# Performance work log

Measured on AMD Instinct MI355X. Metric: run time of the kernel, lower is better.

The kernel has to match this reference:

```python
import jax, jax.numpy as jnp
import numpy as np
import math

B, L, H, E = 4, 2048, 8, 64


def setup_inputs() -> dict:
    key = jax.random.key(0)
    kq, kk, kv, ks = jax.random.split(key, 4)
    return {
        "queries": jax.random.normal(kq, (B, L, H, E), dtype=jnp.float32),
        "keys": jax.random.normal(kk, (B, L, H, E), dtype=jnp.float32),
        "values": jax.random.normal(kv, (B, L, H, E), dtype=jnp.float32),
        "sigma": jax.random.normal(ks, (B, L, H), dtype=jnp.float32),
    }


def reference(queries, keys, values, sigma):
    Bq, Lq, Hq, Eq = queries.shape
    scale = 1.0 / math.sqrt(Eq)
    # QK^T: [B, H, L, S]
    scores = jnp.einsum("blhe,bshe->bhls", queries, keys)
    # triangular causal mask (mask_flag=True, attn_mask=None)
    causal = jnp.triu(jnp.ones((Lq, Lq), dtype=bool), k=1)
    scores = jnp.where(causal[None, None], -jnp.inf, scores)
    attn = scale * scores
    series = jax.nn.softmax(attn, axis=-1)  # dropout p=0.0 -> identity
    # sigma: [B, L, H] -> [B, H, L]
    sig = jnp.transpose(sigma, (0, 2, 1))
    sig = jax.nn.sigmoid(sig * 5.0) + 1e-5
    sig = jnp.power(3.0, sig) - 1.0
    sig = jnp.broadcast_to(sig[..., None], (Bq, Hq, Lq, Lq))  # [B,H,L,L]
    # |i - j| distances
    idx = jnp.arange(Lq, dtype=jnp.float32)
    dist = jnp.abs(idx[:, None] - idx[None, :])  # [L, L]
    prior = (1.0 / (math.sqrt(2.0 * math.pi) * sig)) * jnp.exp(
        -(dist[None, None] ** 2) / (2.0 * sig ** 2)
    )
    V = jnp.einsum("bhls,bshd->blhd", series, values)
    return V, series, prior, sig
```

## Files before the change

kernel.cpp:

```cpp
#include <hip/hip_runtime.h>
#include <math.h>

#define BB 4
#define LL 2048
#define HH 8
#define EE 64
#define TM 64
#define TN 64
#define SH 72

typedef _Float16 half4v __attribute__((ext_vector_type(4)));
typedef _Float16 half8v __attribute__((ext_vector_type(8)));
typedef float floatx4 __attribute__((ext_vector_type(4)));

static constexpr float SCALE = 0.125f;
static constexpr float LN3 = 1.0986122886681098f;
static constexpr float INV_SQRT_2PI = 0.3989422804014327f;
static constexpr size_t NMAT = (size_t)BB * HH * LL * LL;
static constexpr size_t SERIES_BASE = (size_t)BB * LL * HH * EE;
static constexpr size_t PRIOR_BASE = SERIES_BASE + NMAT;
static constexpr size_t SIG_BASE = PRIOR_BASE + NMAT;

__global__ __launch_bounds__(256, 8)
void prior_sig_fill(const float* __restrict__ sgg, float* __restrict__ out) {
  const int lane = threadIdx.x & 63;
  const int wv = (blockIdx.x << 2) | (threadIdx.x >> 6);
  const int nw = gridDim.x << 2;
  const int totalRows = BB * HH * LL;
  for (int row = wv; row < totalRows; row += nw) {
    const int bh = row >> 11;
    const int i = row & (LL - 1);
    const int b = bh >> 3, h = bh & 7;
    float sg = sgg[((size_t)b * LL + i) * HH + h];
    float sd = 1.0f / (1.0f + __expf(-5.0f * sg)) + 1e-5f;
    float sv = expm1f(sd * LN3);
    float iv = INV_SQRT_2PI / sv;
    float c2 = 0.5f / (sv * sv);
    const size_t roff = ((size_t)bh * LL + i) * LL;
    const floatx4 s4 = {sv, sv, sv, sv};
    const float fi = (float)i;
#pragma unroll
    for (int it = 0; it < 8; ++it) {
      int j = (it << 8) + (lane << 2);
      float d0 = fi - (float)j;
      float d1 = d0 - 1.0f, d2 = d0 - 2.0f, d3 = d0 - 3.0f;
      floatx4 pr;
      pr.x = iv * __expf(-d0 * d0 * c2);
      pr.y = iv * __expf(-d1 * d1 * c2);
      pr.z = iv * __expf(-d2 * d2 * c2);
      pr.w = iv * __expf(-d3 * d3 * c2);
      __builtin_nontemporal_store(pr, (floatx4*)&out[PRIOR_BASE + roff + j]);
      __builtin_nontemporal_store(s4, (floatx4*)&out[SIG_BASE + roff + j]);
    }
    const int jz = ((i >> 6) + 1) << 6;
    const floatx4 z = {0.f, 0.f, 0.f, 0.f};
    for (int j = jz + (lane << 2); j < LL; j += 256) {
      __builtin_nontemporal_store(z, (floatx4*)&out[SERIES_BASE + roff + j]);
    }
  }
}

__global__ __launch_bounds__(256, 2)
void anomaly_attn(const float* __restrict__ qg,
                  const float* __restrict__ kg,
                  const float* __restrict__ vg,
                  float* __restrict__ out) {
  __shared__ __attribute__((aligned(16))) _Float16 Qh[TM * SH];
  __shared__ __attribute__((aligned(16))) _Float16 Kh[TN * SH];
  __shared__ __attribute__((aligned(16))) _Float16 Vt[EE * SH];
  __shared__ __attribute__((aligned(16))) _Float16 Ph[TM * SH];

  const int t = threadIdx.x;
  const int lane = t & 63;
  const int w = t >> 6;
  const int quad = lane >> 4;
  const int l15 = lane & 15;
  const int bh = blockIdx.y;
  const int b = bh >> 3, h = bh & 7;
  const float4* q4 = (const float4*)qg;
  const float4* k4 = (const float4*)kg;
  const float4* v4 = (const float4*)vg;

  for (int half = 0; half < 2; ++half) {
    const int rt = half ? (31 - (int)blockIdx.x) : (int)blockIdx.x;
    const int i0 = rt * TM;
    const int nt = rt + 1;
    __syncthreads();

#pragma unroll
    for (int it = 0; it < 4; ++it) {
      int idx = t + 256 * it;
      int r = idx >> 4, c = idx & 15;
      float4 qv = q4[(((size_t)b * LL + i0 + r) * HH + h) * 16 + c];
      half4v hq = {(_Float16)qv.x, (_Float16)qv.y, (_Float16)qv.z, (_Float16)qv.w};
      *(half4v*)&Qh[r * SH + c * 4] = hq;
    }

    float lsum[4] = {0.f, 0.f, 0.f, 0.f};
    for (int jt = 0; jt < nt; ++jt) {
      const int j0 = jt * TN;
      __syncthreads();
#pragma unroll
      for (int it = 0; it < 4; ++it) {
        int idx = t + 256 * it;
        int r = idx >> 4, c = idx & 15;
        float4 kv = k4[(((size_t)b * LL + j0 + r) * HH + h) * 16 + c];
        half4v hk = {(_Float16)kv.x, (_Float16)kv.y, (_Float16)kv.z, (_Float16)kv.w};
        *(half4v*)&Kh[r * SH + c * 4] = hk;
      }
      __syncthreads();
      floatx4 acc[4] = {{0.f, 0.f, 0.f, 0.f}, {0.f, 0.f, 0.f, 0.f},
                        {0.f, 0.f, 0.f, 0.f}, {0.f, 0.f, 0.f, 0.f}};
#pragma unroll
      for (int ks = 0; ks < 2; ++ks) {
        half8v a = *(half8v*)&Qh[(w * 16 + l15) * SH + ks * 32 + quad * 8];
#pragma unroll
        for (int f = 0; f < 4; ++f) {
          half8v bf = *(half8v*)&Kh[(f * 16 + l15) * SH + ks * 32 + quad * 8];
          acc[f] = __builtin_amdgcn_mfma_f32_16x16x32_f16(a, bf, acc[f], 0, 0, 0);
        }
      }
#pragma unroll
      for (int f = 0; f < 4; ++f) {
        int j = j0 + f * 16 + l15;
#pragma unroll
        for (int r = 0; r < 4; ++r) {
          int i = i0 + w * 16 + quad * 4 + r;
          lsum[r] += (j <= i) ? __expf(acc[f][r] * SCALE) : 0.f;
        }
      }
    }
#pragma unroll
    for (int r = 0; r < 4; ++r) {
      lsum[r] += __shfl_xor(lsum[r], 1);
      lsum[r] += __shfl_xor(lsum[r], 2);
      lsum[r] += __shfl_xor(lsum[r], 4);
      lsum[r] += __shfl_xor(lsum[r], 8);
    }
    float linv[4];
#pragma unroll
    for (int r = 0; r < 4; ++r) linv[r] = 1.0f / lsum[r];

    floatx4 Oacc[4] = {{0.f, 0.f, 0.f, 0.f}, {0.f, 0.f, 0.f, 0.f},
                       {0.f, 0.f, 0.f, 0.f}, {0.f, 0.f, 0.f, 0.f}};
    for (int jt = 0; jt < nt; ++jt) {
      const int j0 = jt * TN;
      __syncthreads();
#pragma unroll
      for (int it = 0; it < 4; ++it) {
        int idx = t + 256 * it;
        int r = idx >> 4, c = idx & 15;
        float4 kv = k4[(((size_t)b * LL + j0 + r) * HH + h) * 16 + c];
        half4v hk = {(_Float16)kv.x, (_Float16)kv.y, (_Float16)kv.z, (_Float16)kv.w};
        *(half4v*)&Kh[r * SH + c * 4] = hk;
      }
      {
        const int tx = t & 15, ty = t >> 4;
        float4 vv[4];
#pragma unroll
        for (int rr = 0; rr < 4; ++rr)
          vv[rr] = v4[(((size_t)b * LL + j0 + ty * 4 + rr) * HH + h) * 16 + tx];
#pragma unroll
        for (int c = 0; c < 4; ++c) {
          float e0 = c == 0 ? vv[0].x : c == 1 ? vv[0].y : c == 2 ? vv[0].z : vv[0].w;
          float e1 = c == 0 ? vv[1].x : c == 1 ? vv[1].y : c == 2 ? vv[1].z : vv[1].w;
          float e2 = c == 0 ? vv[2].x : c == 1 ? vv[2].y : c == 2 ? vv[2].z : vv[2].w;
          float e3 = c == 0 ? vv[3].x : c == 1 ? vv[3].y : c == 2 ? vv[3].z : vv[3].w;
          half4v hv = {(_Float16)e0, (_Float16)e1, (_Float16)e2, (_Float16)e3};
          *(half4v*)&Vt[(tx * 4 + c) * SH + ty * 4] = hv;
        }
      }
      __syncthreads();
      floatx4 acc[4] = {{0.f, 0.f, 0.f, 0.f}, {0.f, 0.f, 0.f, 0.f},
                        {0.f, 0.f, 0.f, 0.f}, {0.f, 0.f, 0.f, 0.f}};
#pragma unroll
      for (int ks = 0; ks < 2; ++ks) {
        half8v a = *(half8v*)&Qh[(w * 16 + l15) * SH + ks * 32 + quad * 8];
#pragma unroll
        for (int f = 0; f < 4; ++f) {
          half8v bf = *(half8v*)&Kh[(f * 16 + l15) * SH + ks * 32 + quad * 8];
          acc[f] = __builtin_amdgcn_mfma_f32_16x16x32_f16(a, bf, acc[f], 0, 0, 0);
        }
      }
#pragma unroll
      for (int f = 0; f < 4; ++f) {
        int j = j0 + f * 16 + l15;
#pragma unroll
        for (int r = 0; r < 4; ++r) {
          int i = i0 + w * 16 + quad * 4 + r;
          float p = (j <= i) ? __expf(acc[f][r] * SCALE) * linv[r] : 0.f;
          Ph[(w * 16 + quad * 4 + r) * SH + f * 16 + l15] = (_Float16)p;
        }
      }
      __syncthreads();
#pragma unroll
      for (int rnd = 0; rnd < 2; ++rnd) {
        int idx = t + 256 * rnd;
        int r = idx >> 3, c8 = idx & 7;
        half8v p = *(half8v*)&Ph[r * SH + c8 * 8];
        floatx4 lo = {(float)p[0], (float)p[1], (float)p[2], (float)p[3]};
        floatx4 hi = {(float)p[4], (float)p[5], (float)p[6], (float)p[7]};
        size_t off = SERIES_BASE + ((size_t)bh * LL + i0 + r) * LL + j0 + c8 * 8;
        __builtin_nontemporal_store(lo, (floatx4*)&out[off]);
        __builtin_nontemporal_store(hi, (floatx4*)&out[off + 4]);
      }
#pragma unroll
      for (int ks = 0; ks < 2; ++ks) {
        half8v a = *(half8v*)&Ph[(w * 16 + l15) * SH + ks * 32 + quad * 8];
#pragma unroll
        for (int f = 0; f < 4; ++f) {
          half8v bv = *(half8v*)&Vt[(f * 16 + l15) * SH + ks * 32 + quad * 8];
          Oacc[f] = __builtin_amdgcn_mfma_f32_16x16x32_f16(a, bv, Oacc[f], 0, 0, 0);
        }
      }
    }
#pragma unroll
    for (int f = 0; f < 4; ++f) {
#pragma unroll
      for (int r = 0; r < 4; ++r) {
        int i = i0 + w * 16 + quad * 4 + r;
        out[(((size_t)b * LL + i) * HH + h) * EE + f * 16 + l15] = Oacc[f][r];
      }
    }
  }
}

extern "C" void kernel_launch(void* const* d_in, const int* in_sizes, int n_in,
                              void* d_out, int out_size, void* d_ws, size_t ws_size,
                              hipStream_t stream) {
  const float* q = (const float*)d_in[0];
  const float* k = (const float*)d_in[1];
  const float* v = (const float*)d_in[2];
  const float* sg = (const float*)d_in[3];
  float* out = (float*)d_out;
  prior_sig_fill<<<dim3(2048), 256, 0, stream>>>(sg, out);
  dim3 grid(LL / TM / 2, BB * HH);
  anomaly_attn<<<grid, 256, 0, stream>>>(q, k, v, out);
}
```

Baseline: 1.763 ms.

## Fuse two-pass softmax into single pass with deferred series normalization

Replaces the two-pass scheme, which recomputed QK^T once for row sums and again for probabilities, with a single pass. That pass accumulates row sums, writes unnormalized probabilities to the series output, and normalizes the PV accumulator at the end. A tail loop then reads the series rows back from global memory, scales them by the inverse row sum and stores them again. The kernel now launches one block per row tile instead of pairing tiles for load balance, raises the occupancy hint, and runs the prior fill after the attention kernel. This removes the duplicated QK matmul and exp work but adds a full read-modify-write of the causal half of the series matrix and loses the triangular load balancing.

```diff
diff --git a/kernel.cpp b/kernel.cpp
--- a/kernel.cpp
+++ b/kernel.cpp
@@ -60,7 +60,7 @@
   }
 }
 
-__global__ __launch_bounds__(256, 2)
+__global__ __launch_bounds__(256, 4)
 void anomaly_attn(const float* __restrict__ qg,
                   const float* __restrict__ kg,
                   const float* __restrict__ vg,
@@ -69,6 +69,7 @@
   __shared__ __attribute__((aligned(16))) _Float16 Kh[TN * SH];
   __shared__ __attribute__((aligned(16))) _Float16 Vt[EE * SH];
   __shared__ __attribute__((aligned(16))) _Float16 Ph[TM * SH];
+  __shared__ float s_linv[TM];
 
   const int t = threadIdx.x;
   const int lane = t & 63;
@@ -77,150 +78,136 @@
   const int l15 = lane & 15;
   const int bh = blockIdx.y;
   const int b = bh >> 3, h = bh & 7;
+  const int rt = blockIdx.x;
+  const int i0 = rt * TM;
+  const int nt = rt + 1;
   const float4* q4 = (const float4*)qg;
   const float4* k4 = (const float4*)kg;
   const float4* v4 = (const float4*)vg;
 
-  for (int half = 0; half < 2; ++half) {
-    const int rt = half ? (31 - (int)blockIdx.x) : (int)blockIdx.x;
-    const int i0 = rt * TM;
-    const int nt = rt + 1;
+#pragma unroll
+  for (int it = 0; it < 4; ++it) {
+    int idx = t + 256 * it;
+    int r = idx >> 4, c = idx & 15;
+    float4 qv = q4[(((size_t)b * LL + i0 + r) * HH + h) * 16 + c];
+    half4v hq = {(_Float16)qv.x, (_Float16)qv.y, (_Float16)qv.z, (_Float16)qv.w};
+    *(half4v*)&Qh[r * SH + c * 4] = hq;
+  }
+
+  float lsum[4] = {0.f, 0.f, 0.f, 0.f};
+  floatx4 Oacc[4] = {{0.f, 0.f, 0.f, 0.f}, {0.f, 0.f, 0.f, 0.f},
+                     {0.f, 0.f, 0.f, 0.f}, {0.f, 0.f, 0.f, 0.f}};
+
+  for (int jt = 0; jt < nt; ++jt) {
+    const int j0 = jt * TN;
     __syncthreads();
-
 #pragma unroll
     for (int it = 0; it < 4; ++it) {
       int idx = t + 256 * it;
       int r = idx >> 4, c = idx & 15;
-      float4 qv = q4[(((size_t)b * LL + i0 + r) * HH + h) * 16 + c];
-      half4v hq = {(_Float16)qv.x, (_Float16)qv.y, (_Float16)qv.z, (_Float16)qv.w};
-      *(half4v*)&Qh[r * SH + c * 4] = hq;
-    }
-
-    float lsum[4] = {0.f, 0.f, 0.f, 0.f};
-    for (int jt = 0; jt < nt; ++jt) {
-      const int j0 = jt * TN;
-      __syncthreads();
-#pragma unroll
-      for (int it = 0; it < 4; ++it) {
-        int idx = t + 256 * it;
-        int r = idx >> 4, c = idx & 15;
-        float4 kv = k4[(((size_t)b * LL + j0 + r) * HH + h) * 16 + c];
-        half4v hk = {(_Float16)kv.x, (_Float16)kv.y, (_Float16)kv.z, (_Float16)kv.w};
-        *(half4v*)&Kh[r * SH + c * 4] = hk;
-      }
-      __syncthreads();
-      floatx4 acc[4] = {{0.f, 0.f, 0.f, 0.f}, {0.f, 0.f, 0.f, 0.f},
-                        {0.f, 0.f, 0.f, 0.f}, {0.f, 0.f, 0.f, 0.f}};
-#pragma unroll
-      for (int ks = 0; ks < 2; ++ks) {
-        half8v a = *(half8v*)&Qh[(w * 16 + l15) * SH + ks * 32 + quad * 8];
-#pragma unroll
-        for (int f = 0; f < 4; ++f) {
-          half8v bf = *(half8v*)&Kh[(f * 16 + l15) * SH + ks * 32 + quad * 8];
-          acc[f] = __builtin_amdgcn_mfma_f32_16x16x32_f16(a, bf, acc[f], 0, 0, 0);
-        }
-      }
+      float4 kv = k4[(((size_t)b * LL + j0 + r) * HH + h) * 16 + c];
+      half4v hk = {(_Float16)kv.x, (_Float16)kv.y, (_Float16)kv.z, (_Float16)kv.w};
+      *(half4v*)&Kh[r * SH + c * 4] = hk;
+    }
+    {
+      const int tx = t & 15, ty = t >> 4;
+      float4 vv[4];
+#pragma unroll
+      for (int rr = 0; rr < 4; ++rr)
+        vv[rr] = v4[(((size_t)b * LL + j0 + ty * 4 + rr) * HH + h) * 16 + tx];
+#pragma unroll
+      for (int c = 0; c < 4; ++c) {
+        float e0 = c == 0 ? vv[0].x : c == 1 ? vv[0].y : c == 2 ? vv[0].z : vv[0].w;
+        float e1 = c == 0 ? vv[1].x : c == 1 ? vv[1].y : c == 2 ? vv[1].z : vv[1].w;
+        float e2 = c == 0 ? vv[2].x : c == 1 ? vv[2].y : c == 2 ? vv[2].z : vv[2].w;
+        float e3 = c == 0 ? vv[3].x : c == 1 ? vv[3].y : c == 2 ? vv[3].z : vv[3].w;
+        half4v hv = {(_Float16)e0, (_Float16)e1, (_Float16)e2, (_Float16)e3};
+        *(half4v*)&Vt[(tx * 4 + c) * SH + ty * 4] = hv;
+      }
+    }
+    __syncthreads();
+
+    floatx4 acc[4] = {{0.f, 0.f, 0.f, 0.f}, {0.f, 0.f, 0.f, 0.f},
+                      {0.f, 0.f, 0.f, 0.f}, {0.f, 0.f, 0.f, 0.f}};
+#pragma unroll
+    for (int ks = 0; ks < 2; ++ks) {
+      half8v a = *(half8v*)&Qh[(w * 16 + l15) * SH + ks * 32 + quad * 8];
 #pragma unroll
       for (int f = 0; f < 4; ++f) {
-        int j = j0 + f * 16 + l15;
-#pragma unroll
-        for (int r = 0; r < 4; ++r) {
-          int i = i0 + w * 16 + quad * 4 + r;
-          lsum[r] += (j <= i) ? __expf(acc[f][r] * SCALE) : 0.f;
-        }
-      }
-    }
-#pragma unroll
-    for (int r = 0; r < 4; ++r) {
-      lsum[r] += __shfl_xor(lsum[r], 1);
-      lsum[r] += __shfl_xor(lsum[r], 2);
-      lsum[r] += __shfl_xor(lsum[r], 4);
-      lsum[r] += __shfl_xor(lsum[r], 8);
-    }
-    float linv[4];
-#pragma unroll
-    for (int r = 0; r < 4; ++r) linv[r] = 1.0f / lsum[r];
-
-    floatx4 Oacc[4] = {{0.f, 0.f, 0.f, 0.f}, {0.f, 0.f, 0.f, 0.f},
-                       {0.f, 0.f, 0.f, 0.f}, {0.f, 0.f, 0.f, 0.f}};
-    for (int jt = 0; jt < nt; ++jt) {
-      const int j0 = jt * TN;
-      __syncthreads();
-#pragma unroll
-      for (int it = 0; it < 4; ++it) {
-        int idx = t + 256 * it;
-        int r = idx >> 4, c = idx & 15;
-        float4 kv = k4[(((size_t)b * LL + j0 + r) * HH + h) * 16 + c];
-        half4v hk = {(_Float16)kv.x, (_Float16)kv.y, (_Float16)kv.z, (_Float16)kv.w};
-        *(half4v*)&Kh[r * SH + c * 4] = hk;
-      }
-      {
-        const int tx = t & 15, ty = t >> 4;
-        float4 vv[4];
-#pragma unroll
-        for (int rr = 0; rr < 4; ++rr)
-          vv[rr] = v4[(((size_t)b * LL + j0 + ty * 4 + rr) * HH + h) * 16 + tx];
-#pragma unroll
-        for (int c = 0; c < 4; ++c) {
-          float e0 = c == 0 ? vv[0].x : c == 1 ? vv[0].y : c == 2 ? vv[0].z : vv[0].w;
-          float e1 = c == 0 ? vv[1].x : c == 1 ? vv[1].y : c == 2 ? vv[1].z : vv[1].w;
-          float e2 = c == 0 ? vv[2].x : c == 1 ? vv[2].y : c == 2 ? vv[2].z : vv[2].w;
-          float e3 = c == 0 ? vv[3].x : c == 1 ? vv[3].y : c == 2 ? vv[3].z : vv[3].w;
-          half4v hv = {(_Float16)e0, (_Float16)e1, (_Float16)e2, (_Float16)e3};
-          *(half4v*)&Vt[(tx * 4 + c) * SH + ty * 4] = hv;
-        }
-      }
-      __syncthreads();
-      floatx4 acc[4] = {{0.f, 0.f, 0.f, 0.f}, {0.f, 0.f, 0.f, 0.f},
-                        {0.f, 0.f, 0.f, 0.f}, {0.f, 0.f, 0.f, 0.f}};
-#pragma unroll
-      for (int ks = 0; ks < 2; ++ks) {
-        half8v a = *(half8v*)&Qh[(w * 16 + l15) * SH + ks * 32 + quad * 8];
-#pragma unroll
-        for (int f = 0; f < 4; ++f) {
-          half8v bf = *(half8v*)&Kh[(f * 16 + l15) * SH + ks * 32 + quad * 8];
-          acc[f] = __builtin_amdgcn_mfma_f32_16x16x32_f16(a, bf, acc[f], 0, 0, 0);
-        }
-      }
-#pragma unroll
-      for (int f = 0; f < 4; ++f) {
-        int j = j0 + f * 16 + l15;
-#pragma unroll
-        for (int r = 0; r < 4; ++r) {
-          int i = i0 + w * 16 + quad * 4 + r;
-          float p = (j <= i) ? __expf(acc[f][r] * SCALE) * linv[r] : 0.f;
-          Ph[(w * 16 + quad * 4 + r) * SH + f * 16 + l15] = (_Float16)p;
-        }
-      }
-      __syncthreads();
-#pragma unroll
-      for (int rnd = 0; rnd < 2; ++rnd) {
-        int idx = t + 256 * rnd;
-        int r = idx >> 3, c8 = idx & 7;
-        half8v p = *(half8v*)&Ph[r * SH + c8 * 8];
-        floatx4 lo = {(float)p[0], (float)p[1], (float)p[2], (float)p[3]};
-        floatx4 hi = {(float)p[4], (float)p[5], (float)p[6], (float)p[7]};
-        size_t off = SERIES_BASE + ((size_t)bh * LL + i0 + r) * LL + j0 + c8 * 8;
-        __builtin_nontemporal_store(lo, (floatx4*)&out[off]);
-        __builtin_nontemporal_store(hi, (floatx4*)&out[off + 4]);
-      }
-#pragma unroll
-      for (int ks = 0; ks < 2; ++ks) {
-        half8v a = *(half8v*)&Ph[(w * 16 + l15) * SH + ks * 32 + quad * 8];
-#pragma unroll
-        for (int f = 0; f < 4; ++f) {
-          half8v bv = *(half8v*)&Vt[(f * 16 + l15) * SH + ks * 32 + quad * 8];
-          Oacc[f] = __builtin_amdgcn_mfma_f32_16x16x32_f16(a, bv, Oacc[f], 0, 0, 0);
-        }
+        half8v bf = *(half8v*)&Kh[(f * 16 + l15) * SH + ks * 32 + quad * 8];
+        acc[f] = __builtin_amdgcn_mfma_f32_16x16x32_f16(a, bf, acc[f], 0, 0, 0);
       }
     }
 #pragma unroll
     for (int f = 0; f < 4; ++f) {
+      int j = j0 + f * 16 + l15;
 #pragma unroll
       for (int r = 0; r < 4; ++r) {
         int i = i0 + w * 16 + quad * 4 + r;
-        out[(((size_t)b * LL + i) * HH + h) * EE + f * 16 + l15] = Oacc[f][r];
-      }
+        float p = (j <= i) ? __expf(acc[f][r] * SCALE) : 0.f;
+        lsum[r] += p;
+        Ph[(w * 16 + quad * 4 + r) * SH + f * 16 + l15] = (_Float16)p;
+      }
+    }
+#pragma unroll
+    for (int rnd = 0; rnd < 2; ++rnd) {
+      int row = w * 16 + rnd * 8 + (lane >> 3);
+      int c8 = lane & 7;
+      half8v p = *(half8v*)&Ph[row * SH + c8 * 8];
+      floatx4 lo = {(float)p[0], (float)p[1], (float)p[2], (float)p[3]};
+      floatx4 hi = {(float)p[4], (float)p[5], (float)p[6], (float)p[7]};
+      size_t off = SERIES_BASE + ((size_t)bh * LL + i0 + row) * LL + j0 + c8 * 8;
+      *(floatx4*)&out[off] = lo;
+      *(floatx4*)&out[off + 4] = hi;
+    }
+#pragma unroll
+    for (int ks = 0; ks < 2; ++ks) {
+      half8v a = *(half8v*)&Ph[(w * 16 + l15) * SH + ks * 32 + quad * 8];
+#pragma unroll
+      for (int f = 0; f < 4; ++f) {
+        half8v bv = *(half8v*)&Vt[(f * 16 + l15) * SH + ks * 32 + quad * 8];
+        Oacc[f] = __builtin_amdgcn_mfma_f32_16x16x32_f16(a, bv, Oacc[f], 0, 0, 0);
+      }
+    }
+  }
+
+#pragma unroll
+  for (int r = 0; r < 4; ++r) {
+    lsum[r] += __shfl_xor(lsum[r], 1);
+    lsum[r] += __shfl_xor(lsum[r], 2);
+    lsum[r] += __shfl_xor(lsum[r], 4);
+    lsum[r] += __shfl_xor(lsum[r], 8);
+  }
+  float linv[4];
+#pragma unroll
+  for (int r = 0; r < 4; ++r) linv[r] = 1.0f / lsum[r];
+
+#pragma unroll
+  for (int f = 0; f < 4; ++f) {
+#pragma unroll
+    for (int r = 0; r < 4; ++r) {
+      int i = i0 + w * 16 + quad * 4 + r;
+      out[(((size_t)b * LL + i) * HH + h) * EE + f * 16 + l15] = Oacc[f][r] * linv[r];
+    }
+  }
+
+  if (l15 == 0) {
+#pragma unroll
+    for (int r = 0; r < 4; ++r) s_linv[w * 16 + quad * 4 + r] = linv[r];
+  }
+  __syncthreads();
+
+  const int ncol4 = nt * 16;
+  const int rsub = t >> 6;
+  const int cl = t & 63;
+  for (int rr = 0; rr < 16; ++rr) {
+    int row = rr * 4 + rsub;
+    float li = s_linv[row];
+    size_t base = SERIES_BASE + ((size_t)bh * LL + i0 + row) * LL;
+    for (int c = cl; c < ncol4; c += 64) {
+      floatx4 v = *(const floatx4*)&out[base + c * 4];
+      v *= li;
+      __builtin_nontemporal_store(v, (floatx4*)&out[base + c * 4]);
     }
   }
 }
@@ -233,7 +220,7 @@
   const float* v = (const float*)d_in[2];
   const float* sg = (const float*)d_in[3];
   float* out = (float*)d_out;
+  dim3 grid(LL / TM, BB * HH);
+  anomaly_attn<<<grid, 256, 0, stream>>>(q, k, v, out);
   prior_sig_fill<<<dim3(2048), 256, 0, stream>>>(sg, out);
-  dim3 grid(LL / TM / 2, BB * HH);
-  anomaly_attn<<<grid, 256, 0, stream>>>(q, k, v, out);
 }
```

Measured after the change: 1.920 ms. 8.9% more time.

## Fuse prior/sigma fill and series zero-fill into attention kernel

Applied to the files above, without the earlier changes.

Removes the separate prior_sig_fill launch and moves its work into the attention kernel. Each block computes per-row sigma constants into shared memory, then writes chunks of the prior, sigma and upper-triangle zero regions between its QK and PV tile iterations, with any leftover chunks written at the end. Block indices are remapped so each block owns one (b,h) pair and a complementary pair of row tiles. The intent is to overlap the large output store traffic with matrix compute, at the cost of more register and code pressure in the attention kernel and uneven store work per iteration.

```diff
diff --git a/kernel.cpp b/kernel.cpp
--- a/kernel.cpp
+++ b/kernel.cpp
@@ -21,68 +21,92 @@
 static constexpr size_t PRIOR_BASE = SERIES_BASE + NMAT;
 static constexpr size_t SIG_BASE = PRIOR_BASE + NMAT;
 
-__global__ __launch_bounds__(256, 8)
-void prior_sig_fill(const float* __restrict__ sgg, float* __restrict__ out) {
-  const int lane = threadIdx.x & 63;
-  const int wv = (blockIdx.x << 2) | (threadIdx.x >> 6);
-  const int nw = gridDim.x << 2;
-  const int totalRows = BB * HH * LL;
-  for (int row = wv; row < totalRows; row += nw) {
-    const int bh = row >> 11;
-    const int i = row & (LL - 1);
-    const int b = bh >> 3, h = bh & 7;
-    float sg = sgg[((size_t)b * LL + i) * HH + h];
-    float sd = 1.0f / (1.0f + __expf(-5.0f * sg)) + 1e-5f;
-    float sv = expm1f(sd * LN3);
-    float iv = INV_SQRT_2PI / sv;
-    float c2 = 0.5f / (sv * sv);
-    const size_t roff = ((size_t)bh * LL + i) * LL;
-    const floatx4 s4 = {sv, sv, sv, sv};
-    const float fi = (float)i;
-#pragma unroll
-    for (int it = 0; it < 8; ++it) {
-      int j = (it << 8) + (lane << 2);
-      float d0 = fi - (float)j;
-      float d1 = d0 - 1.0f, d2 = d0 - 2.0f, d3 = d0 - 3.0f;
-      floatx4 pr;
-      pr.x = iv * __expf(-d0 * d0 * c2);
-      pr.y = iv * __expf(-d1 * d1 * c2);
-      pr.z = iv * __expf(-d2 * d2 * c2);
-      pr.w = iv * __expf(-d3 * d3 * c2);
-      __builtin_nontemporal_store(pr, (floatx4*)&out[PRIOR_BASE + roff + j]);
-      __builtin_nontemporal_store(s4, (floatx4*)&out[SIG_BASE + roff + j]);
-    }
-    const int jz = ((i >> 6) + 1) << 6;
-    const floatx4 z = {0.f, 0.f, 0.f, 0.f};
-    for (int j = jz + (lane << 2); j < LL; j += 256) {
-      __builtin_nontemporal_store(z, (floatx4*)&out[SERIES_BASE + roff + j]);
-    }
-  }
-}
-
 __global__ __launch_bounds__(256, 2)
 void anomaly_attn(const float* __restrict__ qg,
                   const float* __restrict__ kg,
                   const float* __restrict__ vg,
+                  const float* __restrict__ sgg,
                   float* __restrict__ out) {
   __shared__ __attribute__((aligned(16))) _Float16 Qh[TM * SH];
   __shared__ __attribute__((aligned(16))) _Float16 Kh[TN * SH];
   __shared__ __attribute__((aligned(16))) _Float16 Vt[EE * SH];
   __shared__ __attribute__((aligned(16))) _Float16 Ph[TM * SH];
+  __shared__ float s_sigv[2 * TM], s_pinv[2 * TM], s_c2[2 * TM];
 
   const int t = threadIdx.x;
   const int lane = t & 63;
   const int w = t >> 6;
   const int quad = lane >> 4;
   const int l15 = lane & 15;
-  const int bh = blockIdx.y;
+
+  const int rx = blockIdx.x;
+  const int ry = blockIdx.y;
+  const int bh = (rx & 7) | ((ry & 3) << 3);
+  const int st = (rx >> 3) | ((ry >> 2) << 1);
   const int b = bh >> 3, h = bh & 7;
+  const int rt0 = st, rt1 = 31 - st;
+  const int i00 = rt0 * TM, i01 = rt1 * TM;
+
   const float4* q4 = (const float4*)qg;
   const float4* k4 = (const float4*)kg;
   const float4* v4 = (const float4*)vg;
 
+  if (t < 128) {
+    int hf = t >> 6, rr = t & 63;
+    int irow = (hf ? i01 : i00) + rr;
+    float sg = sgg[((size_t)b * LL + irow) * HH + h];
+    float sd = 1.0f / (1.0f + __expf(-5.0f * sg)) + 1e-5f;
+    float sv = expm1f(sd * LN3);
+    s_sigv[t] = sv;
+    s_pinv[t] = INV_SQRT_2PI / sv;
+    s_c2[t] = 0.5f / (sv * sv);
+  }
+
+  int cq = 0;
+  const int z0 = 31 - st;
+  auto write_chunk = [&](int c) {
+    if (c < 64) {
+      const int hf = c >> 5;
+      const int jc = c & 31;
+      const int i0c = hf ? i01 : i00;
+#pragma unroll
+      for (int u = 0; u < 4; ++u) {
+        int idx = t + 256 * u;
+        int rr = idx >> 4, cc = idx & 15;
+        int sidx = hf * 64 + rr;
+        float iv = s_pinv[sidx], c2 = s_c2[sidx], sv = s_sigv[sidx];
+        float fi = (float)(i0c + rr);
+        float d0 = fi - (float)(jc * 64 + cc * 4);
+        float d1 = d0 - 1.0f, d2 = d0 - 2.0f, d3 = d0 - 3.0f;
+        floatx4 pr;
+        pr.x = iv * __expf(-d0 * d0 * c2);
+        pr.y = iv * __expf(-d1 * d1 * c2);
+        pr.z = iv * __expf(-d2 * d2 * c2);
+        pr.w = iv * __expf(-d3 * d3 * c2);
+        size_t off = ((size_t)bh * LL + (i0c + rr)) * LL + jc * 64 + cc * 4;
+        __builtin_nontemporal_store(pr, (floatx4*)&out[PRIOR_BASE + off]);
+        floatx4 s4 = {sv, sv, sv, sv};
+        __builtin_nontemporal_store(s4, (floatx4*)&out[SIG_BASE + off]);
+      }
+    } else {
+      int z = c - 64;
+      int hf, jc;
+      if (z < z0) { hf = 0; jc = st + 1 + z; }
+      else        { hf = 1; jc = z + 1; }
+      const int i0c = hf ? i01 : i00;
+      const floatx4 zz = {0.f, 0.f, 0.f, 0.f};
+#pragma unroll
+      for (int u = 0; u < 4; ++u) {
+        int idx = t + 256 * u;
+        int rr = idx >> 4, cc = idx & 15;
+        size_t off = SERIES_BASE + ((size_t)bh * LL + (i0c + rr)) * LL + jc * 64 + cc * 4;
+        __builtin_nontemporal_store(zz, (floatx4*)&out[off]);
+      }
+    }
+  };
+
   for (int half = 0; half < 2; ++half) {
-    const int rt = half ? (31 - (int)blockIdx.x) : (int)blockIdx.x;
+    const int rt = half ? rt1 : rt0;
     const int i0 = rt * TM;
     const int nt = rt + 1;
     __syncthreads();
@@ -129,6 +153,8 @@
           lsum[r] += (j <= i) ? __expf(acc[f][r] * SCALE) : 0.f;
         }
       }
+      if (cq < 95) write_chunk(cq++);
+      if (cq < 95) write_chunk(cq++);
     }
 #pragma unroll
     for (int r = 0; r < 4; ++r) {
@@ -213,6 +239,8 @@
           Oacc[f] = __builtin_amdgcn_mfma_f32_16x16x32_f16(a, bv, Oacc[f], 0, 0, 0);
         }
       }
+      if (cq < 95) write_chunk(cq++);
+      if (cq < 95) write_chunk(cq++);
     }
 #pragma unroll
     for (int f = 0; f < 4; ++f) {
@@ -223,6 +251,7 @@
       }
     }
   }
+  while (cq < 95) write_chunk(cq++);
 }
 
 extern "C" void kernel_launch(void* const* d_in, const int* in_sizes, int n_in,
@@ -233,7 +262,6 @@
   const float* v = (const float*)d_in[2];
   const float* sg = (const float*)d_in[3];
   float* out = (float*)d_out;
-  prior_sig_fill<<<dim3(2048), 256, 0, stream>>>(sg, out);
   dim3 grid(LL / TM / 2, BB * HH);
-  anomaly_attn<<<grid, 256, 0, stream>>>(q, k, v, out);
+  anomaly_attn<<<grid, 256, 0, stream>>>(q, k, v, sg, out);
 }
```

Result: slower. 1.822 ms (+3.4%).
